# Kernel optimization log

Measured on AMD Instinct MI355X. Metric: run time of the kernel, lower is better.

The kernel has to match this reference:

```python
import jax, jax.numpy as jnp
import numpy as np

ITERS = 2


def setup_inputs() -> dict:
    key = jax.random.key(0)
    ks = jax.random.split(key, 10)
    B, R, F, I = 16, 1024, 1024, 1024
    s = 0.05  # param init scale for numerical stability
    return {
        "features": jax.random.normal(ks[0], (B, R, F), jnp.float32),
        "boxes": jax.random.uniform(ks[1], (B, R, 4), jnp.float32),
        "fc_box_w": jax.random.normal(ks[2], (F, 4), jnp.float32) * s,
        "fc_box_b": jax.random.normal(ks[3], (F,), jnp.float32) * s,
        "fc_input_w": jax.random.normal(ks[4], (I, F), jnp.float32) * s,
        "fc_input_b": jax.random.normal(ks[5], (I,), jnp.float32) * s,
        "w_ih": jax.random.normal(ks[6], (3 * F, I), jnp.float32) * s,
        "w_hh": jax.random.normal(ks[7], (3 * F, F), jnp.float32) * s,
        "b_ih": jax.random.normal(ks[8], (3 * F,), jnp.float32) * s,
        "b_hh": jax.random.normal(ks[9], (3 * F,), jnp.float32) * s,
    }


def reference(features, boxes, fc_box_w, fc_box_b, fc_input_w, fc_input_b,
              w_ih, w_hh, b_ih, b_hh):
    B, R, F = features.shape
    # fc_box(boxes): [B, R, F] (same every iteration -> hoisted, math identical)
    box_feat = jnp.einsum('brk,fk->brf', boxes, fc_box_w) + fc_box_b
    denom = jnp.float32(max(1, R - 1))
    h = features
    for _ in range(ITERS):
        # fc_input(relu(h * box_feat)): [B, R, I]
        x = jnp.einsum('brf,if->bri', jax.nn.relu(h * box_feat), fc_input_w) + fc_input_b
        # per-image sum-aggregation, broadcast-subtract, normalize
        inp = (jnp.sum(x, axis=1, keepdims=True) - x) / denom
        # torch.nn.GRUCell math
        gi = jnp.einsum('bri,gi->brg', inp, w_ih) + b_ih   # [B, R, 3F]
        gh = jnp.einsum('brf,gf->brg', h, w_hh) + b_hh     # [B, R, 3F]
        i_r, i_z, i_n = jnp.split(gi, 3, axis=-1)
        h_r, h_z, h_n = jnp.split(gh, 3, axis=-1)
        r = jax.nn.sigmoid(i_r + h_r)
        z = jax.nn.sigmoid(i_z + h_z)
        n = jnp.tanh(i_n + r * h_n)
        h = (1.0 - z) * n + z * h
    # torch.cat over images -> [B*R, F]
    return h.reshape(B * R, F)
```

## Files before the change

### kernel.cpp

```cpp
#include <hip/hip_runtime.h>
#include <cstdint>


typedef unsigned short u16;
typedef short   vshort8 __attribute__((ext_vector_type(8)));
typedef float   vfloat4 __attribute__((ext_vector_type(4)));
typedef u16     vu16x4  __attribute__((ext_vector_type(4)));
typedef u16     vu16x8  __attribute__((ext_vector_type(8)));

#define DEVI __device__ __forceinline__

DEVI u16 f2bf(float f) {
  uint32_t u = __float_as_uint(f);
  u += 0x7FFFu + ((u >> 16) & 1u);
  return (u16)(u >> 16);
}
DEVI float bf2f(u16 h) { return __uint_as_float(((uint32_t)h) << 16); }
DEVI float sigm(float x) { return 1.0f / (1.0f + __expf(-x)); }
DEVI float tanh_(float x) {
  float ax = fabsf(x);
  float e  = __expf(-2.0f * ax);
  float t  = (1.0f - e) / (1.0f + e);
  return x < 0.0f ? -t : t;
}
DEVI vfloat4 mfma_bf16(vshort8 a, vshort8 b, vfloat4 c) {
  return __builtin_amdgcn_mfma_f32_16x16x32_bf16(a, b, c, 0, 0, 0);
}
DEVI void gl16(const void* g, void* l) {
  __builtin_amdgcn_global_load_lds(
      (__attribute__((address_space(1))) void*)(void*)g,
      (__attribute__((address_space(3))) void*)l, 16, 0, 0);
}


__global__ __launch_bounds__(256) void k_cvt4(const float* __restrict__ in,
                                              u16* __restrict__ outp, int n4) {
  int i = blockIdx.x * 256 + threadIdx.x;
  if (i >= n4) return;
  const float4 v = ((const float4*)in)[i];
  vu16x4 o; o[0] = f2bf(v.x); o[1] = f2bf(v.y); o[2] = f2bf(v.z); o[3] = f2bf(v.w);
  *(vu16x4*)(outp + (size_t)i * 4) = o;
}

__global__ __launch_bounds__(256) void k_wcat(const float* __restrict__ wih,
                                              const float* __restrict__ whh,
                                              u16* __restrict__ wc) {
  int i = blockIdx.x * 256 + threadIdx.x;
  const int g = i >> 9, j4 = (i & 511) << 2;
  float4 v; float s;
  if (j4 < 1024) { v = *(const float4*)&wih[((size_t)g << 10) + j4]; s = -1.0f / 1023.0f; }
  else           { v = *(const float4*)&whh[((size_t)g << 10) + (j4 - 1024)]; s = 1.0f; }
  vu16x4 o;
  o[0] = f2bf(v.x * s); o[1] = f2bf(v.y * s); o[2] = f2bf(v.z * s); o[3] = f2bf(v.w * s);
  *(vu16x4*)(wc + (size_t)g * 2048 + j4) = o;
}

__global__ __launch_bounds__(256) void k_wn(const float* __restrict__ wih,
                                            const float* __restrict__ whh,
                                            u16* __restrict__ wni, u16* __restrict__ wnh) {
  int i = blockIdx.x * 256 + threadIdx.x;
  const int gg = i >> 8, j4 = (i & 255) << 2;
  const size_t src = ((size_t)(2048 + gg) << 10) + j4;
  const size_t dst = ((size_t)gg << 10) + j4;
  const float4 a = *(const float4*)&wih[src];
  const float4 b = *(const float4*)&whh[src];
  const float s = -1.0f / 1023.0f;
  vu16x4 oi, oh;
  oi[0] = f2bf(a.x * s); oi[1] = f2bf(a.y * s); oi[2] = f2bf(a.z * s); oi[3] = f2bf(a.w * s);
  oh[0] = f2bf(b.x);     oh[1] = f2bf(b.y);     oh[2] = f2bf(b.z);     oh[3] = f2bf(b.w);
  *(vu16x4*)(wni + dst) = oi;
  *(vu16x4*)(wnh + dst) = oh;
}

__global__ __launch_bounds__(256) void k_apass(const float* __restrict__ H,
                                               const float* __restrict__ boxes,
                                               const float* __restrict__ bw, const float* __restrict__ bb,
                                               u16* __restrict__ A) {
  const int T = blockIdx.x * 256 + threadIdx.x;
  const int m = T >> 7;
  const int f0 = (T & 127) << 3;
  const size_t o = ((size_t)m << 10) + f0;
  const float4 bx = *(const float4*)&boxes[(size_t)m << 2];
  const float4 h0 = *(const float4*)&H[o];
  const float4 h1 = *(const float4*)&H[o + 4];
  const float hv[8] = {h0.x, h0.y, h0.z, h0.w, h1.x, h1.y, h1.z, h1.w};
  vu16x8 oa;
#pragma unroll
  for (int j = 0; j < 8; ++j) {
    const int f = f0 + j;
    const float4 wv = *(const float4*)&bw[(size_t)f << 2];
    const float bfv = bb[f] + bx.x * wv.x + bx.y * wv.y + bx.z * wv.z + bx.w * wv.w;
    float a = hv[j] * bfv;
    oa[j] = f2bf(a > 0.0f ? a : 0.0f);
  }
  *(vu16x8*)(A + o) = oa;
}


__global__ __launch_bounds__(256) void k_sred1(const u16* __restrict__ X,
                                               float* __restrict__ part) {
  const int b = blockIdx.x, ch = blockIdx.y;
  const int r0 = ch << 5;
  const int c4 = threadIdx.x << 2;
  float a0 = 0, a1 = 0, a2 = 0, a3 = 0;
  for (int r = 0; r < 32; ++r) {
    const size_t base = ((size_t)((b << 10) + r0 + r) << 10) + c4;
    const vu16x4 v = *(const vu16x4*)(X + base);
    a0 += bf2f(v[0]); a1 += bf2f(v[1]); a2 += bf2f(v[2]); a3 += bf2f(v[3]);
  }
  const size_t pb = ((size_t)((b << 5) + ch) << 10) + c4;
  float4 o; o.x = a0; o.y = a1; o.z = a2; o.w = a3;
  *(float4*)(part + pb) = o;
}

__global__ __launch_bounds__(256) void k_sred2(const float* __restrict__ part, float* __restrict__ s) {
  const int i = blockIdx.x * 256 + threadIdx.x;
  const int b = i >> 10, col = i & 1023;
  float a = 0;
  for (int ch = 0; ch < 32; ++ch) a += part[((size_t)((b << 5) + ch) << 10) + col];
  s[i] = a;
}

__global__ __launch_bounds__(256) void k_t(const float* __restrict__ s, const float* __restrict__ wih,
                                           float* __restrict__ t) {
  const int g = blockIdx.x;
  const int tid = threadIdx.x, lane = tid & 63, w = tid >> 6;
  float acc[16];
#pragma unroll
  for (int b = 0; b < 16; ++b) acc[b] = 0.0f;
  for (int i = tid; i < 1024; i += 256) {
    const float wv = wih[((size_t)g << 10) + i];
#pragma unroll
    for (int b = 0; b < 16; ++b) acc[b] += s[(b << 10) + i] * wv;
  }
  __shared__ float red[16][4];
#pragma unroll
  for (int b = 0; b < 16; ++b) {
    float v = acc[b];
    for (int off = 32; off > 0; off >>= 1) v += __shfl_down(v, off);
    if (lane == 0) red[b][w] = v;
  }
  __syncthreads();
  if (tid < 16) t[tid * 3072 + g] = red[tid][0] + red[tid][1] + red[tid][2] + red[tid][3];
}


__global__ __launch_bounds__(256) void k_gemm_x(
    const u16* __restrict__ A, const u16* __restrict__ B,
    const float* __restrict__ bias, u16* __restrict__ X) {
  __shared__ u16 As[4096], Bs[4096];
  const int tid = threadIdx.x, w = tid >> 6, lane = tid & 63;
  const int bm0 = (blockIdx.x >> 3) << 7;
  const int bn0 = (blockIdx.x & 7) << 7;
  const int wr = w >> 1, wc = w & 1;
  const int row16 = lane & 15, k8 = (lane >> 4) << 3;
  vfloat4 acc[4][4] = {};

  for (int kt = 0; kt < 32; ++kt) {
    const int k0 = kt << 5;
    __syncthreads();
#pragma unroll
    for (int r = 0; r < 2; ++r) {
      const int cbase = (w << 6) + (r << 8);
      const int c = cbase + lane;
      const int rowT = c >> 2, col8 = (c & 3) << 3;
      const int eo = cbase << 3;
      gl16(A + (size_t)(bm0 + rowT) * 1024 + (k0 + col8), As + eo);
      gl16(B + (size_t)(bn0 + rowT) * 1024 + (k0 + col8), Bs + eo);
    }
    __syncthreads();
    vshort8 af[4], bf[4];
#pragma unroll
    for (int mf = 0; mf < 4; ++mf)
      af[mf] = *(const vshort8*)(As + (((wr << 6) + (mf << 4) + row16) << 5) + k8);
#pragma unroll
    for (int nf = 0; nf < 4; ++nf)
      bf[nf] = *(const vshort8*)(Bs + (((wc << 6) + (nf << 4) + row16) << 5) + k8);
#pragma unroll
    for (int mf = 0; mf < 4; ++mf)
#pragma unroll
      for (int nf = 0; nf < 4; ++nf)
        acc[mf][nf] = mfma_bf16(af[mf], bf[nf], acc[mf][nf]);
  }
#pragma unroll
  for (int mf = 0; mf < 4; ++mf)
#pragma unroll
    for (int nf = 0; nf < 4; ++nf) {
      const int gcol = bn0 + (wc << 6) + (nf << 4) + row16;
      const int grow0 = bm0 + (wr << 6) + (mf << 4) + ((lane >> 4) << 2);
      const float bv = bias[gcol];
#pragma unroll
      for (int rg = 0; rg < 4; ++rg)
        X[(size_t)(grow0 + rg) * 1024 + gcol] = f2bf(acc[mf][nf][rg] + bv);
    }
}

__global__ __launch_bounds__(512) void k_gates(
    const u16* __restrict__ X, const u16* __restrict__ Hbf,
    const float* __restrict__ Hsrc,
    const u16* __restrict__ Wcat, const u16* __restrict__ Wni, const u16* __restrict__ Wnh,
    const float* __restrict__ tbuf, const float* __restrict__ bih, const float* __restrict__ bhh,
    float* __restrict__ out) {
  __shared__ u16 As[4096], Br[4096], Bz[4096], Bn[4096];
  const int tid = threadIdx.x, w = tid >> 6, lane = tid & 63;
  const int cpx = gridDim.x >> 3;
  const int swz = (blockIdx.x & 7) * cpx + (blockIdx.x >> 3);
  const int bm0 = (swz >> 3) << 7;
  const int bn0 = (swz & 7) << 7;
  const int wm = w >> 2, wn = w & 3;
  const int row16 = lane & 15, k8 = (lane >> 4) << 3;
  const int cbase = w << 6;
  const int c = cbase + lane;
  const int rowT = c >> 2, col8 = (c & 3) << 3;
  const int eo = cbase << 3;

  vfloat4 ar[4][2] = {}, az[4][2] = {}, ani[4][2] = {}, anh[4][2] = {};

#pragma unroll 1
  for (int kt = 0; kt < 32; ++kt) {
    const int kk = kt << 5;
    __syncthreads();
    gl16(X    + (size_t)(bm0 + rowT) * 1024 + kk + col8, As + eo);
    gl16(Wcat + (size_t)(bn0 + rowT) * 2048 + kk + col8, Br + eo);
    gl16(Wcat + (size_t)(1024 + bn0 + rowT) * 2048 + kk + col8, Bz + eo);
    gl16(Wni  + (size_t)(bn0 + rowT) * 1024 + kk + col8, Bn + eo);
    __syncthreads();
    vshort8 af[4], br[2], bz[2], bn[2];
#pragma unroll
    for (int mf = 0; mf < 4; ++mf)
      af[mf] = *(const vshort8*)(As + (((wm << 6) + (mf << 4) + row16) << 5) + k8);
#pragma unroll
    for (int nf = 0; nf < 2; ++nf) {
      const int rB = (((wn << 5) + (nf << 4) + row16) << 5) + k8;
      br[nf] = *(const vshort8*)(Br + rB);
      bz[nf] = *(const vshort8*)(Bz + rB);
      bn[nf] = *(const vshort8*)(Bn + rB);
    }
#pragma unroll
    for (int mf = 0; mf < 4; ++mf)
#pragma unroll
      for (int nf = 0; nf < 2; ++nf) {
        ar[mf][nf]  = mfma_bf16(af[mf], br[nf], ar[mf][nf]);
        az[mf][nf]  = mfma_bf16(af[mf], bz[nf], az[mf][nf]);
        ani[mf][nf] = mfma_bf16(af[mf], bn[nf], ani[mf][nf]);
      }
  }
#pragma unroll 1
  for (int kt = 0; kt < 32; ++kt) {
    const int kk = kt << 5;
    const int k0 = 1024 + kk;
    __syncthreads();
    gl16(Hbf  + (size_t)(bm0 + rowT) * 1024 + kk + col8, As + eo);
    gl16(Wcat + (size_t)(bn0 + rowT) * 2048 + k0 + col8, Br + eo);
    gl16(Wcat + (size_t)(1024 + bn0 + rowT) * 2048 + k0 + col8, Bz + eo);
    gl16(Wnh  + (size_t)(bn0 + rowT) * 1024 + kk + col8, Bn + eo);
    __syncthreads();
    vshort8 af[4], br[2], bz[2], bn[2];
#pragma unroll
    for (int mf = 0; mf < 4; ++mf)
      af[mf] = *(const vshort8*)(As + (((wm << 6) + (mf << 4) + row16) << 5) + k8);
#pragma unroll
    for (int nf = 0; nf < 2; ++nf) {
      const int rB = (((wn << 5) + (nf << 4) + row16) << 5) + k8;
      br[nf] = *(const vshort8*)(Br + rB);
      bz[nf] = *(const vshort8*)(Bz + rB);
      bn[nf] = *(const vshort8*)(Bn + rB);
    }
#pragma unroll
    for (int mf = 0; mf < 4; ++mf)
#pragma unroll
      for (int nf = 0; nf < 2; ++nf) {
        ar[mf][nf]  = mfma_bf16(af[mf], br[nf], ar[mf][nf]);
        az[mf][nf]  = mfma_bf16(af[mf], bz[nf], az[mf][nf]);
        anh[mf][nf] = mfma_bf16(af[mf], bn[nf], anh[mf][nf]);
      }
  }

  const float inv = 1.0f / 1023.0f;
  const int b = bm0 >> 10;
#pragma unroll
  for (int nf = 0; nf < 2; ++nf) {
    const int gcol = bn0 + (wn << 5) + (nf << 4) + row16;
    const float cr = tbuf[b * 3072 + gcol] * inv + bih[gcol] + bhh[gcol];
    const float cz = tbuf[b * 3072 + 1024 + gcol] * inv + bih[1024 + gcol] + bhh[1024 + gcol];
    const float ci = tbuf[b * 3072 + 2048 + gcol] * inv + bih[2048 + gcol];
    const float ch = bhh[2048 + gcol];
#pragma unroll
    for (int mf = 0; mf < 4; ++mf) {
      const int grow0 = bm0 + (wm << 6) + (mf << 4) + ((lane >> 4) << 2);
#pragma unroll
      for (int rg = 0; rg < 4; ++rg) {
        const size_t o = (size_t)(grow0 + rg) * 1024 + gcol;
        const float rv  = sigm(ar[mf][nf][rg] + cr);
        const float zv  = sigm(az[mf][nf][rg] + cz);
        const float i_n = ani[mf][nf][rg] + ci;
        const float h_n = anh[mf][nf][rg] + ch;
        const float nv  = tanh_(i_n + rv * h_n);
        out[o] = (1.0f - zv) * nv + zv * Hsrc[o];
      }
    }
  }
}


extern "C" void kernel_launch(void* const* d_in, const int* in_sizes, int n_in,
                              void* d_out, int out_size, void* d_ws, size_t ws_size,
                              hipStream_t stream) {
  const float* features   = (const float*)d_in[0];
  const float* boxes      = (const float*)d_in[1];
  const float* fc_box_w   = (const float*)d_in[2];
  const float* fc_box_b   = (const float*)d_in[3];
  const float* fc_input_w = (const float*)d_in[4];
  const float* fc_input_b = (const float*)d_in[5];
  const float* w_ih       = (const float*)d_in[6];
  const float* w_hh       = (const float*)d_in[7];
  const float* b_ih       = (const float*)d_in[8];
  const float* b_hh       = (const float*)d_in[9];
  float* out = (float*)d_out;

  u16 *fcw, *wcat, *wni, *wnh, *A, *X, *Hbf;
  float *part, *sbuf, *tbuf;
  int NB = 16;
  for (;; NB >>= 1) {
    if (NB == 0) return;
    char* base = (char*)d_ws;
    size_t off = 0;
    auto take = [&](size_t bytes) -> char* {
      char* q = base + off;
      off += (bytes + 255) & ~(size_t)255;
      return q;
    };
    const size_t CPLANE = (size_t)NB * 1024 * 1024 * 2;
    fcw  = (u16*)take((size_t)1024 * 1024 * 2);
    wcat = (u16*)take((size_t)2048 * 2048 * 2);
    wni  = (u16*)take((size_t)1024 * 1024 * 2);
    wnh  = (u16*)take((size_t)1024 * 1024 * 2);
    part = (float*)take((size_t)16 * 32 * 1024 * 4);
    sbuf = (float*)take((size_t)16 * 1024 * 4);
    tbuf = (float*)take((size_t)16 * 3072 * 4);
    A    = (u16*)take(CPLANE);
    X    = (u16*)take(CPLANE);
    Hbf  = (u16*)take(CPLANE);
    if (off <= ws_size) break;
  }
  const int NCH = 16 / NB;

  k_cvt4<<<1024, 256, 0, stream>>>(fc_input_w, fcw, 262144);
  k_wcat<<<4096, 256, 0, stream>>>(w_ih, w_hh, wcat);
  k_wn<<<1024, 256, 0, stream>>>(w_ih, w_hh, wni, wnh);

  for (int it = 0; it < 2; ++it) {
    const float* Hfull = it ? (const float*)out : features;
    for (int cc = 0; cc < NCH; ++cc) {
      const size_t m0 = (size_t)cc * NB * 1024;
      const float* Hsrc = Hfull + m0 * 1024;
      k_apass<<<NB * 512, 256, 0, stream>>>(Hsrc, boxes + m0 * 4,
                                            fc_box_w, fc_box_b, A);
      k_gemm_x<<<NB * 64, 256, 0, stream>>>(A, fcw, fc_input_b, X);
      k_sred1<<<dim3(NB, 32), 256, 0, stream>>>(X, part);
      k_sred2<<<NB * 4, 256, 0, stream>>>(part, sbuf);
      k_t<<<3072, 256, 0, stream>>>(sbuf, w_ih, tbuf);
      k_cvt4<<<NB * 1024, 256, 0, stream>>>(Hsrc, Hbf, NB * 262144);
      k_gates<<<NB * 64, 512, 0, stream>>>(X, Hbf, Hsrc, wcat, wni, wnh,
                                           tbuf, b_ih, b_hh, out + m0 * 1024);
    }
  }
}
```

Baseline: 1.038 ms.

## Swizzle LDS tiles in GEMMs and fuse H bf16 conversion into apass

Applies an XOR swizzle to the k-chunk position of the shared-memory tiles in k_gemm_x and k_gates. Global loads pick the permuted source column and MFMA fragment reads use the matching swizzled offset, which is meant to cut LDS bank conflicts. Separately, k_apass now also writes the bf16 copy of H, so the separate k_cvt4 launch and its extra read of H are removed. The swizzle must match between writer and reader, or the GEMM results would be corrupted.

```diff
diff --git a/kernel.cpp b/kernel.cpp
--- a/kernel.cpp
+++ b/kernel.cpp
@@ -75,7 +75,7 @@
 __global__ __launch_bounds__(256) void k_apass(const float* __restrict__ H,
                                                const float* __restrict__ boxes,
                                                const float* __restrict__ bw, const float* __restrict__ bb,
-                                               u16* __restrict__ A) {
+                                               u16* __restrict__ A, u16* __restrict__ Hbf) {
   const int T = blockIdx.x * 256 + threadIdx.x;
   const int m = T >> 7;
   const int f0 = (T & 127) << 3;
@@ -84,7 +84,7 @@
   const float4 h0 = *(const float4*)&H[o];
   const float4 h1 = *(const float4*)&H[o + 4];
   const float hv[8] = {h0.x, h0.y, h0.z, h0.w, h1.x, h1.y, h1.z, h1.w};
-  vu16x8 oa;
+  vu16x8 oa, ohb;
 #pragma unroll
   for (int j = 0; j < 8; ++j) {
     const int f = f0 + j;
@@ -92,8 +92,10 @@
     const float bfv = bb[f] + bx.x * wv.x + bx.y * wv.y + bx.z * wv.z + bx.w * wv.w;
     float a = hv[j] * bfv;
     oa[j] = f2bf(a > 0.0f ? a : 0.0f);
+    ohb[j] = f2bf(hv[j]);
   }
   *(vu16x8*)(A + o) = oa;
+  *(vu16x8*)(Hbf + o) = ohb;
 }
 
 
@@ -153,7 +155,8 @@
   const int bm0 = (blockIdx.x >> 3) << 7;
   const int bn0 = (blockIdx.x & 7) << 7;
   const int wr = w >> 1, wc = w & 1;
-  const int row16 = lane & 15, k8 = (lane >> 4) << 3;
+  const int row16 = lane & 15;
+  const int k8s = (((lane >> 4) ^ ((row16 >> 1) & 3)) << 3);
   vfloat4 acc[4][4] = {};
 
   for (int kt = 0; kt < 32; ++kt) {
@@ -163,7 +166,8 @@
     for (int r = 0; r < 2; ++r) {
       const int cbase = (w << 6) + (r << 8);
       const int c = cbase + lane;
-      const int rowT = c >> 2, col8 = (c & 3) << 3;
+      const int rowT = c >> 2;
+      const int col8 = (((c & 3) ^ ((c >> 3) & 3)) << 3);
       const int eo = cbase << 3;
       gl16(A + (size_t)(bm0 + rowT) * 1024 + (k0 + col8), As + eo);
       gl16(B + (size_t)(bn0 + rowT) * 1024 + (k0 + col8), Bs + eo);
@@ -172,10 +176,10 @@
     vshort8 af[4], bf[4];
 #pragma unroll
     for (int mf = 0; mf < 4; ++mf)
-      af[mf] = *(const vshort8*)(As + (((wr << 6) + (mf << 4) + row16) << 5) + k8);
+      af[mf] = *(const vshort8*)(As + (((wr << 6) + (mf << 4) + row16) << 5) + k8s);
 #pragma unroll
     for (int nf = 0; nf < 4; ++nf)
-      bf[nf] = *(const vshort8*)(Bs + (((wc << 6) + (nf << 4) + row16) << 5) + k8);
+      bf[nf] = *(const vshort8*)(Bs + (((wc << 6) + (nf << 4) + row16) << 5) + k8s);
 #pragma unroll
     for (int mf = 0; mf < 4; ++mf)
 #pragma unroll
@@ -208,10 +212,12 @@
   const int bm0 = (swz >> 3) << 7;
   const int bn0 = (swz & 7) << 7;
   const int wm = w >> 2, wn = w & 3;
-  const int row16 = lane & 15, k8 = (lane >> 4) << 3;
+  const int row16 = lane & 15;
+  const int k8s = (((lane >> 4) ^ ((row16 >> 1) & 3)) << 3);
   const int cbase = w << 6;
   const int c = cbase + lane;
-  const int rowT = c >> 2, col8 = (c & 3) << 3;
+  const int rowT = c >> 2;
+  const int col8 = (((c & 3) ^ ((c >> 3) & 3)) << 3);
   const int eo = cbase << 3;
 
   vfloat4 ar[4][2] = {}, az[4][2] = {}, ani[4][2] = {}, anh[4][2] = {};
@@ -228,10 +234,10 @@
     vshort8 af[4], br[2], bz[2], bn[2];
 #pragma unroll
     for (int mf = 0; mf < 4; ++mf)
-      af[mf] = *(const vshort8*)(As + (((wm << 6) + (mf << 4) + row16) << 5) + k8);
+      af[mf] = *(const vshort8*)(As + (((wm << 6) + (mf << 4) + row16) << 5) + k8s);
 #pragma unroll
     for (int nf = 0; nf < 2; ++nf) {
-      const int rB = (((wn << 5) + (nf << 4) + row16) << 5) + k8;
+      const int rB = (((wn << 5) + (nf << 4) + row16) << 5) + k8s;
       br[nf] = *(const vshort8*)(Br + rB);
       bz[nf] = *(const vshort8*)(Bz + rB);
       bn[nf] = *(const vshort8*)(Bn + rB);
@@ -258,10 +264,10 @@
     vshort8 af[4], br[2], bz[2], bn[2];
 #pragma unroll
     for (int mf = 0; mf < 4; ++mf)
-      af[mf] = *(const vshort8*)(As + (((wm << 6) + (mf << 4) + row16) << 5) + k8);
+      af[mf] = *(const vshort8*)(As + (((wm << 6) + (mf << 4) + row16) << 5) + k8s);
 #pragma unroll
     for (int nf = 0; nf < 2; ++nf) {
-      const int rB = (((wn << 5) + (nf << 4) + row16) << 5) + k8;
+      const int rB = (((wn << 5) + (nf << 4) + row16) << 5) + k8s;
       br[nf] = *(const vshort8*)(Br + rB);
       bz[nf] = *(const vshort8*)(Bz + rB);
       bn[nf] = *(const vshort8*)(Bn + rB);
@@ -355,12 +361,11 @@
       const size_t m0 = (size_t)cc * NB * 1024;
       const float* Hsrc = Hfull + m0 * 1024;
       k_apass<<<NB * 512, 256, 0, stream>>>(Hsrc, boxes + m0 * 4,
-                                            fc_box_w, fc_box_b, A);
+                                            fc_box_w, fc_box_b, A, Hbf);
       k_gemm_x<<<NB * 64, 256, 0, stream>>>(A, fcw, fc_input_b, X);
       k_sred1<<<dim3(NB, 32), 256, 0, stream>>>(X, part);
       k_sred2<<<NB * 4, 256, 0, stream>>>(part, sbuf);
       k_t<<<3072, 256, 0, stream>>>(sbuf, w_ih, tbuf);
-      k_cvt4<<<NB * 1024, 256, 0, stream>>>(Hsrc, Hbf, NB * 262144);
       k_gates<<<NB * 64, 512, 0, stream>>>(X, Hbf, Hsrc, wcat, wni, wnh,
                                            tbuf, b_ih, b_hh, out + m0 * 1024);
     }
```

Result: faster. 979.1 us (-5.6%).
